# Kernel tuning notes

Measured on AMD Instinct MI355X. Metric: run time of the kernel, lower is better.

## Reference

```python
import jax, jax.numpy as jnp
import numpy as np


def setup_inputs() -> dict:
    key = jax.random.key(0)
    k1, k2, k3 = jax.random.split(key, 3)
    N, C, H, W, O = 4, 256, 64, 64, 256
    x = jax.random.normal(k1, (N, C, H, W), jnp.float32)
    # offset per forward signature: [N, H*W, 2*3*3]
    offset = jax.random.normal(k2, (N, H * W, 18), jnp.float32)
    # DeformConv weight [O, C, 3, 3], normal_init std=0.01, bias=False
    weight = jax.random.normal(k3, (O, C, 3, 3), jnp.float32) * 0.01
    return {"x": x, "offset": offset, "weight": weight}


def _deform_conv3x3(x, offset, weight):
    """Deformable conv v1: 3x3, stride 1, padding 1, dilation 1, no bias.
    x: [N,C,H,W]; offset: [N,HW,18] (permuted to [N,18,H,W] as in the module);
    weight: [O,C,3,3].
    """
    N, C, H, W = x.shape
    O = weight.shape[0]
    # module does offset.permute(0,2,1).reshape(N,-1,H,W) -> [N,18,H,W]
    off = offset.transpose(0, 2, 1).reshape(N, 9, 2, H, W)  # (dy,dx) per kernel pos
    dy, dx = off[:, :, 0], off[:, :, 1]                      # [N,9,H,W]

    # base 3x3 kernel offsets (padding=1 keeps the grid centered)
    ky = jnp.array([-1, -1, -1, 0, 0, 0, 1, 1, 1], x.dtype)
    kx = jnp.array([-1, 0, 1, -1, 0, 1, -1, 0, 1], x.dtype)
    hg = jnp.arange(H, dtype=x.dtype)[:, None]  # [H,1]
    wg = jnp.arange(W, dtype=x.dtype)[None, :]  # [1,W]
    py = hg[None, None] + ky[None, :, None, None] + dy  # [N,9,H,W] sample rows
    px = wg[None, None] + kx[None, :, None, None] + dx  # [N,9,H,W] sample cols

    y0 = jnp.floor(py)
    x0 = jnp.floor(px)
    wy = (py - y0)[:, None]  # [N,1,9,H,W]
    wx = (px - x0)[:, None]

    def gather(iy, ix):
        # zero-padded gather: out[n,c,k,h,w] = x[n,c,iy,ix] (0 if out of bounds)
        valid = (iy >= 0) & (iy < H) & (ix >= 0) & (ix < W)
        iyc = jnp.clip(iy, 0, H - 1).astype(jnp.int32)
        ixc = jnp.clip(ix, 0, W - 1).astype(jnp.int32)
        g = jax.vmap(lambda xn, yn, wn: xn[:, yn, wn])(x, iyc, ixc)  # [N,C,9,H,W]
        return g * valid[:, None].astype(x.dtype)

    v00 = gather(y0, x0)
    v01 = gather(y0, x0 + 1)
    v10 = gather(y0 + 1, x0)
    v11 = gather(y0 + 1, x0 + 1)
    # bilinear blend -> sampled columns [N,C,9,H,W]
    val = (v00 * (1 - wy) * (1 - wx) + v01 * (1 - wy) * wx
           + v10 * wy * (1 - wx) + v11 * wy * wx)
    # conv accumulate over channels and kernel positions
    return jnp.einsum('nckhw,ock->nohw', val, weight.reshape(O, C, 9))


def reference(x, offset, weight):
    return _deform_conv3x3(x, offset, weight)
```

## Files before the change

### kernel.cpp

```cpp
#include <hip/hip_runtime.h>
#include <hip/hip_fp16.h>

#define CC 256
#define OO 256
#define HH 64
#define WW 64
#define HWN 4096
#define MPB 64
#define NPB 128
#define KCH 128
#define VST 264
#define WST 136

typedef _Float16 half8 __attribute__((ext_vector_type(8)));
typedef _Float16 half2v __attribute__((ext_vector_type(2)));
typedef float f32x4 __attribute__((ext_vector_type(4)));

__device__ __forceinline__ half2v u2h(unsigned u) {
  half2v h; __builtin_memcpy(&h, &u, 4); return h;
}
__device__ __forceinline__ unsigned h2u(half2v h) {
  unsigned u; __builtin_memcpy(&u, &h, 4); return u;
}
__device__ __forceinline__ unsigned short f2h(float f) {
  _Float16 h = (_Float16)f;
  unsigned short us; __builtin_memcpy(&us, &h, 2);
  return us;
}
__device__ __forceinline__ unsigned dupu(unsigned short us) {
  return ((unsigned)us << 16) | us;
}
__device__ __forceinline__ unsigned pk2(float a, float b) {
  half2v h = {(_Float16)a, (_Float16)b};
  return h2u(h);
}

__global__ __launch_bounds__(256) void prep_kernel(
    const float* __restrict__ x, const float* __restrict__ w,
    _Float16* __restrict__ xt, _Float16* __restrict__ wt) {
  __shared__ float tile[64][65];
  const int bid = blockIdx.x;
  const int tid = threadIdx.x;
  if (bid < 1024) {
    const int n  = bid >> 8;
    const int c0 = ((bid >> 6) & 3) * 64;
    const int s0 = (bid & 63) * 64;
    {
      int r  = tid >> 2;
      int sc = (tid & 3) * 16;
      const float* xp = x + ((size_t)(n * CC + c0 + r)) * HWN + s0 + sc;
      *(float4*)&tile[r][sc]      = *(const float4*)(xp);
      *(float4*)&tile[r][sc + 4]  = *(const float4*)(xp + 4);
      *(float4*)&tile[r][sc + 8]  = *(const float4*)(xp + 8);
      *(float4*)&tile[r][sc + 12] = *(const float4*)(xp + 12);
    }
    __syncthreads();
    {
      int s  = tid >> 2;
      int cg = (tid & 3) * 16;
      uint4 u0, u1;
      u0.x = pk2(tile[cg + 0][s],  tile[cg + 1][s]);
      u0.y = pk2(tile[cg + 2][s],  tile[cg + 3][s]);
      u0.z = pk2(tile[cg + 4][s],  tile[cg + 5][s]);
      u0.w = pk2(tile[cg + 6][s],  tile[cg + 7][s]);
      u1.x = pk2(tile[cg + 8][s],  tile[cg + 9][s]);
      u1.y = pk2(tile[cg + 10][s], tile[cg + 11][s]);
      u1.z = pk2(tile[cg + 12][s], tile[cg + 13][s]);
      u1.w = pk2(tile[cg + 14][s], tile[cg + 15][s]);
      _Float16* op = xt + ((size_t)(n * HWN + s0 + s)) * CC + c0 + cg;
      *(uint4*)(op)     = u0;
      *(uint4*)(op + 8) = u1;
    }
  } else {
    int e = (bid - 1024) * 256 + tid;
    int k = e >> 16;
    int o = (e >> 8) & 255;
    int c = e & 255;
    wt[e] = (_Float16)w[((size_t)o * CC + c) * 9 + k];
  }
}

__global__ __launch_bounds__(256, 2) void deform_mfma_kernel(
    const _Float16* __restrict__ xt,
    const _Float16* __restrict__ wt,
    const float* __restrict__ off,
    float* __restrict__ out) {
  __shared__ __align__(16) _Float16 val_lds[MPB * VST];
  __shared__ __align__(16) _Float16 w_lds[NPB * WST];
  __shared__ ushort4 s_po[MPB * 9];
  __shared__ ushort4 s_pw[MPB * 9];

  const int tid  = threadIdx.x;
  const int lane = tid & 63;
  const int wv   = tid >> 6;
  const int n15  = lane & 15;
  const int quad = lane >> 4;

  const int bx    = blockIdx.x;
  const int nb    = (bx & 7) >> 1;
  const int hw0   = (bx >> 3) * MPB;
  const int obase = (bx & 1) * NPB;

  for (int e = tid; e < MPB * 9; e += 256) {
    int p = e / 9;
    int k = e - p * 9;
    int hw = hw0 + p;
    int h = hw >> 6, w = hw & 63;
    size_t ob = ((size_t)(nb * HWN + hw)) * 18 + 2 * k;
    float2 d = *(const float2*)(off + ob);
    float py = (float)(h + k / 3 - 1) + d.x;
    float px = (float)(w + k % 3 - 1) + d.y;
    float fy = floorf(py), fx = floorf(px);
    int iy = (int)fy, ix = (int)fx;
    float wy = py - fy, wx = px - fx;
    float my0 = ((unsigned)iy       < (unsigned)HH) ? 1.f : 0.f;
    float my1 = ((unsigned)(iy + 1) < (unsigned)HH) ? 1.f : 0.f;
    float mx0 = ((unsigned)ix       < (unsigned)WW) ? 1.f : 0.f;
    float mx1 = ((unsigned)(ix + 1) < (unsigned)WW) ? 1.f : 0.f;
    int iy0 = min(max(iy, 0), HH - 1), iy1 = min(max(iy + 1, 0), HH - 1);
    int ix0 = min(max(ix, 0), WW - 1), ix1 = min(max(ix + 1, 0), WW - 1);
    s_po[e] = make_ushort4((unsigned short)(iy0 * WW + ix0),
                           (unsigned short)(iy0 * WW + ix1),
                           (unsigned short)(iy1 * WW + ix0),
                           (unsigned short)(iy1 * WW + ix1));
    s_pw[e] = make_ushort4(f2h((1.f - wy) * (1.f - wx) * my0 * mx0),
                           f2h((1.f - wy) * wx         * my0 * mx1),
                           f2h(wy         * (1.f - wx) * my1 * mx0),
                           f2h(wy         * wx         * my1 * mx1));
  }

  f32x4 acc[4][2];
#pragma unroll
  for (int a = 0; a < 4; ++a)
#pragma unroll
    for (int b = 0; b < 2; ++b) acc[a][b] = (f32x4){0.f, 0.f, 0.f, 0.f};

  const _Float16* xb = xt + (size_t)nb * HWN * CC;
  const int j = lane & 31;
  const int ph = lane >> 5;

  for (int k = 0; k < 9; ++k) {
    __syncthreads();

#pragma unroll
    for (int i = 0; i < 8; ++i) {
      int p = i * 8 + wv * 2 + ph;
      int idx = p * 9 + k;
      ushort4 o4 = s_po[idx];
      ushort4 hw4 = s_pw[idx];
      half2v w00 = u2h(dupu(hw4.x)), w01 = u2h(dupu(hw4.y));
      half2v w10 = u2h(dupu(hw4.z)), w11 = u2h(dupu(hw4.w));
      const _Float16* cb = xb + (size_t)j * 8;
      uint4 v00 = *(const uint4*)(cb + (size_t)o4.x * CC);
      uint4 v01 = *(const uint4*)(cb + (size_t)o4.y * CC);
      uint4 v10 = *(const uint4*)(cb + (size_t)o4.z * CC);
      uint4 v11 = *(const uint4*)(cb + (size_t)o4.w * CC);
      uint4 r;
      r.x = h2u(u2h(v00.x) * w00 + u2h(v01.x) * w01 + u2h(v10.x) * w10 + u2h(v11.x) * w11);
      r.y = h2u(u2h(v00.y) * w00 + u2h(v01.y) * w01 + u2h(v10.y) * w10 + u2h(v11.y) * w11);
      r.z = h2u(u2h(v00.z) * w00 + u2h(v01.z) * w01 + u2h(v10.z) * w10 + u2h(v11.z) * w11);
      r.w = h2u(u2h(v00.w) * w00 + u2h(v01.w) * w01 + u2h(v10.w) * w10 + u2h(v11.w) * w11);
      *(uint4*)(val_lds + p * VST + j * 8) = r;
    }

    for (int cc = 0; cc < CC / KCH; ++cc) {
      __syncthreads();
      {
        int q = tid & 3;
        int orow = tid >> 2;
#pragma unroll
        for (int rr = 0; rr < 2; ++rr) {
          int o = rr * 64 + orow;
          const uint4* src = (const uint4*)(wt + ((size_t)(k * OO + obase + o)) * CC + cc * KCH + q * 32);
          uint4* dst = (uint4*)(w_lds + o * WST + q * 32);
          dst[0] = src[0];
          dst[1] = src[1];
          dst[2] = src[2];
          dst[3] = src[3];
        }
      }
      __syncthreads();
#pragma unroll
      for (int ks = 0; ks < 4; ++ks) {
        int cbase = cc * KCH + ks * 32;
        half8 afr[4], bfr[2];
#pragma unroll
        for (int mt = 0; mt < 4; ++mt)
          afr[mt] = *(const half8*)(val_lds + (mt * 16 + n15) * VST + cbase + quad * 8);
#pragma unroll
        for (int nt = 0; nt < 2; ++nt)
          bfr[nt] = *(const half8*)(w_lds + (wv * 32 + nt * 16 + n15) * WST + ks * 32 + quad * 8);
#pragma unroll
        for (int mt = 0; mt < 4; ++mt)
#pragma unroll
          for (int nt = 0; nt < 2; ++nt)
            acc[mt][nt] = __builtin_amdgcn_mfma_f32_16x16x32_f16(
                afr[mt], bfr[nt], acc[mt][nt], 0, 0, 0);
      }
    }
  }

#pragma unroll
  for (int mt = 0; mt < 4; ++mt)
#pragma unroll
    for (int nt = 0; nt < 2; ++nt) {
      int o  = obase + wv * 32 + nt * 16 + n15;
      int px = hw0 + mt * 16 + quad * 4;
      *(f32x4*)(out + ((size_t)nb * OO + o) * HWN + px) = acc[mt][nt];
    }
}

extern "C" void kernel_launch(void* const* d_in, const int* in_sizes, int n_in,
                              void* d_out, int out_size, void* d_ws, size_t ws_size,
                              hipStream_t stream) {
  const float* x   = (const float*)d_in[0];
  const float* off = (const float*)d_in[1];
  const float* w   = (const float*)d_in[2];
  float* out = (float*)d_out;

  _Float16* wt = (_Float16*)d_ws;
  _Float16* xt = wt + 589824;

  prep_kernel<<<1024 + 2304, 256, 0, stream>>>(x, w, xt, wt);
  deform_mfma_kernel<<<(4 * HWN / MPB) * (OO / NPB), 256, 0, stream>>>(xt, wt, off, out);
}
```

Measured before the change: 127.3 us.

## Halve pixel tile, read weight fragments from global, and raise occupancy

The main kernel's pixel tile shrinks from 64 to 32 and the weight LDS staging is removed. Each wave now loads its MFMA B fragments straight from the pre-transposed fp16 weights in global memory, which drops the inner channel-chunk loop and its extra barriers. Launch bounds go to 4 blocks per SM, since less LDS and fewer accumulators allow more resident blocks. The prep transpose also writes through the shared tile in transposed order. The cost is less weight reuse per block and more global or L2 weight traffic and gather work per output.

```diff
diff --git a/kernel.cpp b/kernel.cpp
--- a/kernel.cpp
+++ b/kernel.cpp
@@ -6,11 +6,9 @@
 #define HH 64
 #define WW 64
 #define HWN 4096
-#define MPB 64
+#define MPB 32
 #define NPB 128
-#define KCH 128
 #define VST 264
-#define WST 136
 
 typedef _Float16 half8 __attribute__((ext_vector_type(8)));
 typedef _Float16 half2v __attribute__((ext_vector_type(2)));
@@ -49,24 +47,32 @@
       int r  = tid >> 2;
       int sc = (tid & 3) * 16;
       const float* xp = x + ((size_t)(n * CC + c0 + r)) * HWN + s0 + sc;
-      *(float4*)&tile[r][sc]      = *(const float4*)(xp);
-      *(float4*)&tile[r][sc + 4]  = *(const float4*)(xp + 4);
-      *(float4*)&tile[r][sc + 8]  = *(const float4*)(xp + 8);
-      *(float4*)&tile[r][sc + 12] = *(const float4*)(xp + 12);
+      float4 va = *(const float4*)(xp);
+      float4 vb = *(const float4*)(xp + 4);
+      float4 vc = *(const float4*)(xp + 8);
+      float4 vd = *(const float4*)(xp + 12);
+      tile[sc + 0][r]  = va.x;  tile[sc + 1][r]  = va.y;
+      tile[sc + 2][r]  = va.z;  tile[sc + 3][r]  = va.w;
+      tile[sc + 4][r]  = vb.x;  tile[sc + 5][r]  = vb.y;
+      tile[sc + 6][r]  = vb.z;  tile[sc + 7][r]  = vb.w;
+      tile[sc + 8][r]  = vc.x;  tile[sc + 9][r]  = vc.y;
+      tile[sc + 10][r] = vc.z;  tile[sc + 11][r] = vc.w;
+      tile[sc + 12][r] = vd.x;  tile[sc + 13][r] = vd.y;
+      tile[sc + 14][r] = vd.z;  tile[sc + 15][r] = vd.w;
     }
     __syncthreads();
     {
       int s  = tid >> 2;
       int cg = (tid & 3) * 16;
       uint4 u0, u1;
-      u0.x = pk2(tile[cg + 0][s],  tile[cg + 1][s]);
-      u0.y = pk2(tile[cg + 2][s],  tile[cg + 3][s]);
-      u0.z = pk2(tile[cg + 4][s],  tile[cg + 5][s]);
-      u0.w = pk2(tile[cg + 6][s],  tile[cg + 7][s]);
-      u1.x = pk2(tile[cg + 8][s],  tile[cg + 9][s]);
-      u1.y = pk2(tile[cg + 10][s], tile[cg + 11][s]);
-      u1.z = pk2(tile[cg + 12][s], tile[cg + 13][s]);
-      u1.w = pk2(tile[cg + 14][s], tile[cg + 15][s]);
+      u0.x = pk2(tile[s][cg + 0],  tile[s][cg + 1]);
+      u0.y = pk2(tile[s][cg + 2],  tile[s][cg + 3]);
+      u0.z = pk2(tile[s][cg + 4],  tile[s][cg + 5]);
+      u0.w = pk2(tile[s][cg + 6],  tile[s][cg + 7]);
+      u1.x = pk2(tile[s][cg + 8],  tile[s][cg + 9]);
+      u1.y = pk2(tile[s][cg + 10], tile[s][cg + 11]);
+      u1.z = pk2(tile[s][cg + 12], tile[s][cg + 13]);
+      u1.w = pk2(tile[s][cg + 14], tile[s][cg + 15]);
       _Float16* op = xt + ((size_t)(n * HWN + s0 + s)) * CC + c0 + cg;
       *(uint4*)(op)     = u0;
       *(uint4*)(op + 8) = u1;
@@ -80,13 +86,12 @@
   }
 }
 
-__global__ __launch_bounds__(256, 2) void deform_mfma_kernel(
+__global__ __launch_bounds__(256, 4) void deform_mfma_kernel(
     const _Float16* __restrict__ xt,
     const _Float16* __restrict__ wt,
     const float* __restrict__ off,
     float* __restrict__ out) {
   __shared__ __align__(16) _Float16 val_lds[MPB * VST];
-  __shared__ __align__(16) _Float16 w_lds[NPB * WST];
   __shared__ ushort4 s_po[MPB * 9];
   __shared__ ushort4 s_pw[MPB * 9];
 
@@ -129,9 +134,9 @@
                            f2h(wy         * wx         * my1 * mx1));
   }
 
-  f32x4 acc[4][2];
-#pragma unroll
-  for (int a = 0; a < 4; ++a)
+  f32x4 acc[2][2];
+#pragma unroll
+  for (int a = 0; a < 2; ++a)
 #pragma unroll
     for (int b = 0; b < 2; ++b) acc[a][b] = (f32x4){0.f, 0.f, 0.f, 0.f};
 
@@ -143,7 +148,7 @@
     __syncthreads();
 
 #pragma unroll
-    for (int i = 0; i < 8; ++i) {
+    for (int i = 0; i < 4; ++i) {
       int p = i * 8 + wv * 2 + ph;
       int idx = p * 9 + k;
       ushort4 o4 = s_po[idx];
@@ -162,46 +167,29 @@
       r.w = h2u(u2h(v00.w) * w00 + u2h(v01.w) * w01 + u2h(v10.w) * w10 + u2h(v11.w) * w11);
       *(uint4*)(val_lds + p * VST + j * 8) = r;
     }
-
-    for (int cc = 0; cc < CC / KCH; ++cc) {
-      __syncthreads();
-      {
-        int q = tid & 3;
-        int orow = tid >> 2;
-#pragma unroll
-        for (int rr = 0; rr < 2; ++rr) {
-          int o = rr * 64 + orow;
-          const uint4* src = (const uint4*)(wt + ((size_t)(k * OO + obase + o)) * CC + cc * KCH + q * 32);
-          uint4* dst = (uint4*)(w_lds + o * WST + q * 32);
-          dst[0] = src[0];
-          dst[1] = src[1];
-          dst[2] = src[2];
-          dst[3] = src[3];
-        }
-      }
-      __syncthreads();
-#pragma unroll
-      for (int ks = 0; ks < 4; ++ks) {
-        int cbase = cc * KCH + ks * 32;
-        half8 afr[4], bfr[2];
-#pragma unroll
-        for (int mt = 0; mt < 4; ++mt)
-          afr[mt] = *(const half8*)(val_lds + (mt * 16 + n15) * VST + cbase + quad * 8);
+    __syncthreads();
+
+    const _Float16* wb = wt + ((size_t)(k * OO + obase + wv * 32)) * CC;
+#pragma unroll
+    for (int ks = 0; ks < 8; ++ks) {
+      half8 afr[2], bfr[2];
+#pragma unroll
+      for (int mt = 0; mt < 2; ++mt)
+        afr[mt] = *(const half8*)(val_lds + (mt * 16 + n15) * VST + ks * 32 + quad * 8);
+#pragma unroll
+      for (int nt = 0; nt < 2; ++nt)
+        bfr[nt] = *(const half8*)(wb + (size_t)(nt * 16 + n15) * CC + ks * 32 + quad * 8);
+#pragma unroll
+      for (int mt = 0; mt < 2; ++mt)
 #pragma unroll
         for (int nt = 0; nt < 2; ++nt)
-          bfr[nt] = *(const half8*)(w_lds + (wv * 32 + nt * 16 + n15) * WST + ks * 32 + quad * 8);
-#pragma unroll
-        for (int mt = 0; mt < 4; ++mt)
-#pragma unroll
-          for (int nt = 0; nt < 2; ++nt)
-            acc[mt][nt] = __builtin_amdgcn_mfma_f32_16x16x32_f16(
-                afr[mt], bfr[nt], acc[mt][nt], 0, 0, 0);
-      }
+          acc[mt][nt] = __builtin_amdgcn_mfma_f32_16x16x32_f16(
+              afr[mt], bfr[nt], acc[mt][nt], 0, 0, 0);
     }
   }
 
 #pragma unroll
-  for (int mt = 0; mt < 4; ++mt)
+  for (int mt = 0; mt < 2; ++mt)
 #pragma unroll
     for (int nt = 0; nt < 2; ++nt) {
       int o  = obase + wv * 32 + nt * 16 + n15;
```

New measurement: 161.5 us. 26.8% more time.
